# Optimization experiments

Measured on AMD Instinct MI355X. Metric: run time of the kernel, lower is better.

The kernel has to match this reference:

```python
import jax, jax.numpy as jnp
import numpy as np

K = 8  # hardcoded knn_point(8, ...) in the original module


def setup_inputs() -> dict:
    key = jax.random.key(0)
    k1, k2, k3 = jax.random.split(key, 3)
    B, N, S, C = 8, 8192, 2048, 256
    return {
        "xyz": jax.random.normal(k1, (B, 3, N), dtype=jnp.float32),
        "sparse_xyz": jax.random.normal(k2, (B, 3, S), dtype=jnp.float32),
        "sparse_feat": jax.random.normal(k3, (B, C, S), dtype=jnp.float32),
    }


def reference(xyz, sparse_xyz, sparse_feat):
    # xyz: [B,3,N] dense query points; sparse_xyz: [B,3,S]; sparse_feat: [B,C,S]
    B, _, N = xyz.shape
    x = jnp.transpose(xyz, (0, 2, 1))          # [B,N,3]
    sx = jnp.transpose(sparse_xyz, (0, 2, 1))  # [B,S,3]
    sf = jnp.transpose(sparse_feat, (0, 2, 1)) # [B,S,C]

    sqr = (jnp.sum(x * x, axis=-1)[:, :, None]
           + jnp.sum(sx * sx, axis=-1)[:, None, :]
           - 2.0 * jnp.einsum('bnc,bsc->bns', x, sx))

    # K nearest neighbors (smallest distance) -> indices [B,N,K]
    _, idx = jax.lax.top_k(-sqr, K)

    bidx = jnp.arange(B)[:, None, None]
    g_xyz = sx[bidx, idx]                      # gather neighbor coords [B,N,K,3]
    diff = g_xyz - x[:, :, None, :]
    dist = jnp.maximum(jnp.linalg.norm(diff, axis=3), 1e-10)  # [B,N,K]

    inv = 1.0 / dist
    weight = inv / jnp.sum(inv, axis=2, keepdims=True)        # [B,N,K]

    g_feat = sf[bidx, idx]                     # gather neighbor feats [B,N,K,C]
    dense = jnp.sum(weight[..., None] * g_feat, axis=2)       # [B,N,C]
    return jnp.transpose(dense, (0, 2, 1))     # [B,C,N]
```

## Files before the change

### kernel.cpp

```cpp
#include <hip/hip_runtime.h>
#include <hip/hip_fp16.h>

#define BB 8
#define NN 8192
#define SS 2048
#define CC 256
#define KNN 8
#define TOPM 10
#define NCHUNK 4
#define CH (SS / NCHUNK)
#define QPB 64
#define MSTRIDE 41
#define FSTR 12

#define UMIN(a, b) __builtin_elementwise_min(a, b)
#define UMAX(a, b) __builtin_elementwise_max(a, b)
#define UMIN3(a, b, c) UMIN(UMIN(a, b), c)

__device__ __forceinline__ unsigned pack_h2(float a, float b) {
    __half2 h = __halves2half2(__float2half_rn(a), __float2half_rn(b));
    return *reinterpret_cast<unsigned*>(&h);
}
__device__ __forceinline__ float2 unpack_h2(unsigned u) {
    __half2 h = *reinterpret_cast<__half2*>(&u);
    return __half22float2(h);
}

__global__ __launch_bounds__(256, 4) void knn_kernel(
    const float* __restrict__ xyz,
    const float* __restrict__ sxyz,
    unsigned* __restrict__ out_pk)
{
    __shared__ float2   sxy[SS];
    __shared__ float    sz[SS];
    __shared__ unsigned mbuf[QPB * MSTRIDE];

    const int b   = blockIdx.x >> 7;
    const int q0  = (blockIdx.x & 127) * QPB;
    const int tid = threadIdx.x;
    const int wave = tid >> 6;
    const int lane = tid & 63;

    const float* sb = sxyz + (long)b * 3 * SS;
#pragma unroll
    for (int i = 0; i < SS / 256; ++i) {
        int s = tid + i * 256;
        sxy[s] = make_float2(sb[s], sb[SS + s]);
        sz[s]  = sb[2 * SS + s];
    }
    __syncthreads();

    const float* xb = xyz + (long)b * 3 * NN;
    const int n = q0 + lane;
    const float qx = xb[n], qy = xb[NN + n], qz = xb[2 * NN + n];

    unsigned k1[TOPM];
#pragma unroll
    for (int j = 0; j < TOPM; ++j) k1[j] = 0xFFFFFFFFu;

    const int sbase = wave * CH;
#pragma unroll 2
    for (int i = 0; i < CH; i += 2) {
        const int s0 = sbase + i;
        const float4 xy2 = *(const float4*)&sxy[s0];
        const float2 z2  = *(const float2*)&sz[s0];
        float dx0 = xy2.x - qx, dy0 = xy2.y - qy, dz0 = z2.x - qz;
        float dx1 = xy2.z - qx, dy1 = xy2.w - qy, dz1 = z2.y - qz;
        float d0 = fmaf(dx0, dx0, fmaf(dy0, dy0, dz0 * dz0));
        float d1 = fmaf(dx1, dx1, fmaf(dy1, dy1, dz1 * dz1));
        unsigned c0 = (__float_as_uint(d0) & 0xFFFFF800u) | (unsigned)s0;
        unsigned c1 = (__float_as_uint(d1) & 0xFFFFF800u) | (unsigned)(s0 + 1);
        unsigned lo = UMIN(c0, c1), hi = UMAX(c0, c1);
#pragma unroll
        for (int j = TOPM - 1; j >= 2; --j)
            k1[j] = UMIN3(k1[j], UMAX(k1[j - 1], lo), UMAX(k1[j - 2], hi));
        k1[1] = UMIN3(k1[1], UMAX(k1[0], lo), hi);
        k1[0] = UMIN(k1[0], lo);
    }

    {
        unsigned* m1 = &mbuf[lane * MSTRIDE + wave * TOPM];
#pragma unroll
        for (int j = 0; j < TOPM; ++j) m1[j] = k1[j];
    }
    __syncthreads();

    if (tid < QPB) {
        const int nq = q0 + tid;
        const double dqx = (double)xb[nq], dqy = (double)xb[NN + nq], dqz = (double)xb[2 * NN + nq];
        const unsigned* ml = &mbuf[tid * MSTRIDE];

        unsigned long long top[KNN];
#pragma unroll
        for (int j = 0; j < KNN; ++j) top[j] = ~0ull;

        for (int j = 0; j < NCHUNK * TOPM; ++j) {
            unsigned key = ml[j];
            int s = key & 0x7FF;
            float2 pxy = sxy[s];
            float  pz  = sz[s];
            double ex = (double)pxy.x - dqx;
            double ey = (double)pxy.y - dqy;
            double ez = (double)pz - dqz;
            double dd = ex * ex + ey * ey + ez * ez;
            unsigned long long c =
                (((unsigned long long)__double_as_longlong(dd)) & ~0x7FFull) | (unsigned long long)s;
#pragma unroll
            for (int jj = KNN - 1; jj >= 1; --jj)
                top[jj] = UMIN(UMAX(top[jj - 1], c), top[jj]);
            top[0] = UMIN(top[0], c);
        }

        const float fqx = xb[nq], fqy = xb[NN + nq], fqz = xb[2 * NN + nq];
        int   id[KNN];
        float inv[KNN];
        float ssum = 0.f;
#pragma unroll
        for (int k = 0; k < KNN; ++k) {
            id[k] = (int)(top[k] & 0x7FFull);
            float2 pxy = sxy[id[k]];
            float  pz  = sz[id[k]];
            float dx = pxy.x - fqx, dy = pxy.y - fqy, dz = pz - fqz;
            float dv = sqrtf(dx * dx + dy * dy + dz * dz);
            dv = fmaxf(dv, 1e-10f);
            inv[k] = 1.0f / dv;
            ssum += inv[k];
        }
        const float rs = 1.0f / ssum;
        const long base = ((long)b * NN + nq) * KNN;
#pragma unroll
        for (int k = 0; k < KNN; ++k) {
            unsigned hw = (unsigned)__half_as_ushort(__float2half_rn(inv[k] * rs));
            out_pk[base + k] = (hw << 16) | (unsigned)id[k];
        }
    }
}

__global__ __launch_bounds__(256, 2) void accum_kernel(
    const float*    __restrict__ sf,
    const unsigned* __restrict__ pk,
    float* __restrict__ out)
{
    __shared__ unsigned short feat[SS * FSTR];

    const int blk  = blockIdx.x;
    const int b    = blk >> 6;
    const int ct   = (blk >> 1) & 31;
    const int half = blk & 1;
    const int t    = threadIdx.x;
    const int c0   = ct * 8;

    const float* sfb = sf + ((long)b * CC + c0) * SS;
#pragma unroll
    for (int i = 0; i < SS / 256; ++i) {
        int s = i * 256 + t;
        float f[8];
#pragma unroll
        for (int c = 0; c < 8; ++c) f[c] = sfb[(long)c * SS + s];
        uint2 w0 = make_uint2(pack_h2(f[0], f[1]), pack_h2(f[2], f[3]));
        uint2 w1 = make_uint2(pack_h2(f[4], f[5]), pack_h2(f[6], f[7]));
        *(uint2*)&feat[s * FSTR]     = w0;
        *(uint2*)&feat[s * FSTR + 4] = w1;
    }
    __syncthreads();

    const unsigned* pkb = pk + ((long)b * NN + half * 4096) * KNN;
    float* outb = out + ((long)b * CC + c0) * NN + half * 4096;

    for (int it = 0; it < 4096 / 256; ++it) {
        const int nrel = it * 256 + t;
        const uint4 pa = *(const uint4*)(pkb + (long)nrel * KNN);
        const uint4 pb = *(const uint4*)(pkb + (long)nrel * KNN + 4);
        const unsigned pks[8] = {pa.x, pa.y, pa.z, pa.w, pb.x, pb.y, pb.z, pb.w};

        float acc[8];
#pragma unroll
        for (int c = 0; c < 8; ++c) acc[c] = 0.f;

#pragma unroll
        for (int k = 0; k < KNN; ++k) {
            const unsigned p = pks[k];
            const int id = p & 0x7FF;
            const float w = __half2float(__ushort_as_half((unsigned short)(p >> 16)));
            const unsigned short* fp = &feat[id * FSTR];
            uint2 A = *(const uint2*)fp;
            uint2 B = *(const uint2*)(fp + 4);
            float2 f0 = unpack_h2(A.x), f1 = unpack_h2(A.y);
            float2 f2 = unpack_h2(B.x), f3 = unpack_h2(B.y);
            acc[0] = fmaf(w, f0.x, acc[0]);
            acc[1] = fmaf(w, f0.y, acc[1]);
            acc[2] = fmaf(w, f1.x, acc[2]);
            acc[3] = fmaf(w, f1.y, acc[3]);
            acc[4] = fmaf(w, f2.x, acc[4]);
            acc[5] = fmaf(w, f2.y, acc[5]);
            acc[6] = fmaf(w, f3.x, acc[6]);
            acc[7] = fmaf(w, f3.y, acc[7]);
        }

#pragma unroll
        for (int c = 0; c < 8; ++c)
            outb[(long)c * NN + nrel] = acc[c];
    }
}

extern "C" void kernel_launch(void* const* d_in, const int* in_sizes, int n_in,
                              void* d_out, int out_size, void* d_ws, size_t ws_size,
                              hipStream_t stream) {
    const float* xyz  = (const float*)d_in[0];
    const float* sxyz = (const float*)d_in[1];
    const float* sf   = (const float*)d_in[2];
    float* out = (float*)d_out;

    unsigned* pkbuf = (unsigned*)d_ws;

    knn_kernel<<<dim3(BB * NN / QPB), dim3(256), 0, stream>>>(xyz, sxyz, pkbuf);
    accum_kernel<<<dim3(BB * 32 * 2), dim3(256), 0, stream>>>(sf, pkbuf, out);
}
```

Measured before the change: 179.6 us.

## Compute kNN candidate distances with bf16 split-precision MFMA instead of scalar FMAs

The kNN distance scan now runs on matrix cores. Each sparse point and each query is encoded as hi/lo bf16 pairs plus its squared norm, and a 16x16x32 bf16 MFMA yields squared distances for 16 queries by 16 points per step. Each 16-lane group keeps a top-10 list over a strided quarter of the points. Refinement now reads coordinates from global memory instead of LDS. The LDS footprint grows, occupancy drops to 2 blocks per SM, and the bf16 split approximation (with a +0.0625 offset to keep values positive) may change which candidates survive, though exact double-precision refinement of 40 candidates partly guards against that.

Result: slower. 185.4 us (+3.2%).

```diff
diff --git a/kernel.cpp b/kernel.cpp
--- a/kernel.cpp
+++ b/kernel.cpp
@@ -7,8 +7,7 @@
 #define CC 256
 #define KNN 8
 #define TOPM 10
-#define NCHUNK 4
-#define CH (SS / NCHUNK)
+#define NLIST 4
 #define QPB 64
 #define MSTRIDE 41
 #define FSTR 12
@@ -17,6 +16,9 @@
 #define UMAX(a, b) __builtin_elementwise_max(a, b)
 #define UMIN3(a, b, c) UMIN(UMIN(a, b), c)
 
+typedef short bf16x8_t __attribute__((ext_vector_type(8)));
+typedef float f32x4_t __attribute__((ext_vector_type(4)));
+
 __device__ __forceinline__ unsigned pack_h2(float a, float b) {
     __half2 h = __halves2half2(__float2half_rn(a), __float2half_rn(b));
     return *reinterpret_cast<unsigned*>(&h);
@@ -26,81 +28,147 @@
     return __half22float2(h);
 }
 
-__global__ __launch_bounds__(256, 4) void knn_kernel(
+__device__ __forceinline__ unsigned short f2bf(float f) {
+    unsigned u = __float_as_uint(f);
+    u += 0x7FFFu + ((u >> 16) & 1u);
+    return (unsigned short)(u >> 16);
+}
+__device__ __forceinline__ float bf2f(unsigned short h) {
+    return __uint_as_float((unsigned)h << 16);
+}
+
+__device__ __forceinline__ void ins2(unsigned k1[TOPM], unsigned ca, unsigned cb) {
+    unsigned lo = UMIN(ca, cb), hi = UMAX(ca, cb);
+#pragma unroll
+    for (int j = TOPM - 1; j >= 2; --j)
+        k1[j] = UMIN3(k1[j], UMAX(k1[j - 1], lo), UMAX(k1[j - 2], hi));
+    k1[1] = UMIN3(k1[1], UMAX(k1[0], lo), hi);
+    k1[0] = UMIN(k1[0], lo);
+}
+
+__device__ __forceinline__ void ins_step(unsigned k1[TOPM], f32x4_t d, unsigned sbase) {
+    unsigned c0 = (__float_as_uint(d[0]) & 0xFFFFF800u) | sbase;
+    unsigned c1 = (__float_as_uint(d[1]) & 0xFFFFF800u) | (sbase + 1u);
+    unsigned c2 = (__float_as_uint(d[2]) & 0xFFFFF800u) | (sbase + 2u);
+    unsigned c3 = (__float_as_uint(d[3]) & 0xFFFFF800u) | (sbase + 3u);
+    ins2(k1, c0, c1);
+    ins2(k1, c2, c3);
+}
+
+__global__ __launch_bounds__(256, 2) void knn_kernel(
     const float* __restrict__ xyz,
     const float* __restrict__ sxyz,
     unsigned* __restrict__ out_pk)
 {
-    __shared__ float2   sxy[SS];
-    __shared__ float    sz[SS];
+    __shared__ unsigned short tile[SS * 16 + 8];
     __shared__ unsigned mbuf[QPB * MSTRIDE];
 
-    const int b   = blockIdx.x >> 7;
-    const int q0  = (blockIdx.x & 127) * QPB;
-    const int tid = threadIdx.x;
+    const int b    = blockIdx.x >> 7;
+    const int q0   = (blockIdx.x & 127) * QPB;
+    const int tid  = threadIdx.x;
     const int wave = tid >> 6;
     const int lane = tid & 63;
+    const int g    = lane >> 4;
+    const int qi   = lane & 15;
 
     const float* sb = sxyz + (long)b * 3 * SS;
+
 #pragma unroll
     for (int i = 0; i < SS / 256; ++i) {
-        int s = tid + i * 256;
-        sxy[s] = make_float2(sb[s], sb[SS + s]);
-        sz[s]  = sb[2 * SS + s];
+        int s = i * 256 + tid;
+        float px = sb[s], py = sb[SS + s], pz = sb[2 * SS + s];
+        unsigned short xh = f2bf(px); unsigned short xl = f2bf(px - bf2f(xh));
+        unsigned short yh = f2bf(py); unsigned short yl = f2bf(py - bf2f(yh));
+        unsigned short zh = f2bf(pz); unsigned short zl = f2bf(pz - bf2f(zh));
+        float pn = fmaf(px, px, fmaf(py, py, pz * pz));
+        unsigned short nh = f2bf(pn); unsigned short nl = f2bf(pn - bf2f(nh));
+        const unsigned ONE = 0x3F80u;
+        uint4 t0 = make_uint4((unsigned)xh | ((unsigned)xl << 16),
+                              (unsigned)xh | ((unsigned)yh << 16),
+                              (unsigned)yl | ((unsigned)yh << 16),
+                              (unsigned)zh | ((unsigned)zl << 16));
+        uint4 t1 = make_uint4((unsigned)zh | ((unsigned)nh << 16),
+                              (unsigned)nl | (ONE << 16),
+                              ONE, 0u);
+        *(uint4*)&tile[s * 8] = t0;
+        *(uint4*)&tile[SS * 8 + 8 + s * 8] = t1;
+    }
+    if (tid == 0) *(uint4*)&tile[SS * 8] = make_uint4(0u, 0u, 0u, 0u);
+
+    const float* xb = xyz + (long)b * 3 * NN;
+    const int nq = q0 + wave * 16 + qi;
+    const float qx = xb[nq], qy = xb[NN + nq], qz = xb[2 * NN + nq];
+
+    bf16x8_t qf = (bf16x8_t)0;
+    {
+        unsigned short xh = f2bf(qx); float xhf = bf2f(xh);
+        unsigned short yh = f2bf(qy); float yhf = bf2f(yh);
+        unsigned short zh = f2bf(qz); float zhf = bf2f(zh);
+        unsigned short xh2 = f2bf(-2.f * xhf), xl2 = f2bf(-2.f * (qx - xhf));
+        unsigned short yh2 = f2bf(-2.f * yhf), yl2 = f2bf(-2.f * (qy - yhf));
+        unsigned short zh2 = f2bf(-2.f * zhf), zl2 = f2bf(-2.f * (qz - zhf));
+        float qn = fmaf(qx, qx, fmaf(qy, qy, qz * qz)) + 0.0625f;
+        unsigned short nh = f2bf(qn); unsigned short nl = f2bf(qn - bf2f(nh));
+        const short ONE = (short)0x3F80;
+        if (g == 0) {
+            qf[0] = (short)xh2; qf[1] = (short)xh2; qf[2] = (short)xl2;
+            qf[3] = (short)yh2; qf[4] = (short)yh2; qf[5] = (short)yl2;
+            qf[6] = (short)zh2; qf[7] = (short)zh2;
+        } else if (g == 1) {
+            qf[0] = (short)zl2; qf[1] = ONE; qf[2] = ONE;
+            qf[3] = (short)nh;  qf[4] = (short)nl;
+        }
     }
     __syncthreads();
 
-    const float* xb = xyz + (long)b * 3 * NN;
-    const int n = q0 + lane;
-    const float qx = xb[n], qy = xb[NN + n], qz = xb[2 * NN + n];
+    const unsigned short* abase;
+    int astep;
+    if (g == 0)      { abase = &tile[qi * 8];               astep = 128; }
+    else if (g == 1) { abase = &tile[SS * 8 + 8 + qi * 8];  astep = 128; }
+    else             { abase = &tile[SS * 8];               astep = 0;   }
 
     unsigned k1[TOPM];
 #pragma unroll
     for (int j = 0; j < TOPM; ++j) k1[j] = 0xFFFFFFFFu;
 
-    const int sbase = wave * CH;
+    const f32x4_t zacc = {0.f, 0.f, 0.f, 0.f};
+    const unsigned ib4 = (unsigned)(g * 4);
+
+    bf16x8_t af = *(const bf16x8_t*)abase; abase += astep;
+    f32x4_t dc = __builtin_amdgcn_mfma_f32_16x16x32_bf16(af, qf, zacc, 0, 0, 0);
+
 #pragma unroll 2
-    for (int i = 0; i < CH; i += 2) {
-        const int s0 = sbase + i;
-        const float4 xy2 = *(const float4*)&sxy[s0];
-        const float2 z2  = *(const float2*)&sz[s0];
-        float dx0 = xy2.x - qx, dy0 = xy2.y - qy, dz0 = z2.x - qz;
-        float dx1 = xy2.z - qx, dy1 = xy2.w - qy, dz1 = z2.y - qz;
-        float d0 = fmaf(dx0, dx0, fmaf(dy0, dy0, dz0 * dz0));
-        float d1 = fmaf(dx1, dx1, fmaf(dy1, dy1, dz1 * dz1));
-        unsigned c0 = (__float_as_uint(d0) & 0xFFFFF800u) | (unsigned)s0;
-        unsigned c1 = (__float_as_uint(d1) & 0xFFFFF800u) | (unsigned)(s0 + 1);
-        unsigned lo = UMIN(c0, c1), hi = UMAX(c0, c1);
-#pragma unroll
-        for (int j = TOPM - 1; j >= 2; --j)
-            k1[j] = UMIN3(k1[j], UMAX(k1[j - 1], lo), UMAX(k1[j - 2], hi));
-        k1[1] = UMIN3(k1[1], UMAX(k1[0], lo), hi);
-        k1[0] = UMIN(k1[0], lo);
-    }
+    for (int step = 0; step < 127; ++step) {
+        bf16x8_t an = *(const bf16x8_t*)abase; abase += astep;
+        f32x4_t dn = __builtin_amdgcn_mfma_f32_16x16x32_bf16(an, qf, zacc, 0, 0, 0);
+        ins_step(k1, dc, ib4 + (unsigned)(step * 16));
+        dc = dn;
+    }
+    ins_step(k1, dc, ib4 + (unsigned)(127 * 16));
 
     {
-        unsigned* m1 = &mbuf[lane * MSTRIDE + wave * TOPM];
+        unsigned* m1 = &mbuf[(wave * 16 + qi) * MSTRIDE + g * TOPM];
 #pragma unroll
         for (int j = 0; j < TOPM; ++j) m1[j] = k1[j];
     }
     __syncthreads();
 
     if (tid < QPB) {
-        const int nq = q0 + tid;
-        const double dqx = (double)xb[nq], dqy = (double)xb[NN + nq], dqz = (double)xb[2 * NN + nq];
+        const int n2 = q0 + tid;
+        const double dqx = (double)xb[n2], dqy = (double)xb[NN + n2], dqz = (double)xb[2 * NN + n2];
         const unsigned* ml = &mbuf[tid * MSTRIDE];
 
         unsigned long long top[KNN];
 #pragma unroll
         for (int j = 0; j < KNN; ++j) top[j] = ~0ull;
 
-        for (int j = 0; j < NCHUNK * TOPM; ++j) {
+#pragma unroll 4
+        for (int j = 0; j < NLIST * TOPM; ++j) {
             unsigned key = ml[j];
             int s = key & 0x7FF;
-            float2 pxy = sxy[s];
-            float  pz  = sz[s];
-            double ex = (double)pxy.x - dqx;
-            double ey = (double)pxy.y - dqy;
+            float px = sb[s], py = sb[SS + s], pz = sb[2 * SS + s];
+            double ex = (double)px - dqx;
+            double ey = (double)py - dqy;
             double ez = (double)pz - dqz;
             double dd = ex * ex + ey * ey + ez * ez;
             unsigned long long c =
@@ -111,23 +179,22 @@
             top[0] = UMIN(top[0], c);
         }
 
-        const float fqx = xb[nq], fqy = xb[NN + nq], fqz = xb[2 * NN + nq];
+        const float fqx = xb[n2], fqy = xb[NN + n2], fqz = xb[2 * NN + n2];
         int   id[KNN];
         float inv[KNN];
         float ssum = 0.f;
 #pragma unroll
         for (int k = 0; k < KNN; ++k) {
             id[k] = (int)(top[k] & 0x7FFull);
-            float2 pxy = sxy[id[k]];
-            float  pz  = sz[id[k]];
-            float dx = pxy.x - fqx, dy = pxy.y - fqy, dz = pz - fqz;
+            float px = sb[id[k]], py = sb[SS + id[k]], pz = sb[2 * SS + id[k]];
+            float dx = px - fqx, dy = py - fqy, dz = pz - fqz;
             float dv = sqrtf(dx * dx + dy * dy + dz * dz);
             dv = fmaxf(dv, 1e-10f);
             inv[k] = 1.0f / dv;
             ssum += inv[k];
         }
         const float rs = 1.0f / ssum;
-        const long base = ((long)b * NN + nq) * KNN;
+        const long base = ((long)b * NN + n2) * KNN;
 #pragma unroll
         for (int k = 0; k < KNN; ++k) {
             unsigned hw = (unsigned)__half_as_ushort(__float2half_rn(inv[k] * rs));
```
